# Kernel tuning notes

Measured on AMD Instinct MI355X. Metric: run time of the kernel, lower is better.

## Reference

```python
import jax, jax.numpy as jnp
import numpy as np

RADIUS = 0.1
NSAMPLE = 32
NORMALIZE_XYZ = False
USE_XYZ = True


def ball_query(xyz, center_xyz, radius, nsample):
    """xyz: (B,N,3), center_xyz: (B,S,3) -> idx (B,S,nsample) int32.
    For each center, first `nsample` point indices within `radius`;
    slots with no valid point are filled with the first valid index (0 if none)."""
    N = xyz.shape[1]
    # squared distances (B,S,N)
    d2 = jnp.sum((center_xyz[:, :, None, :] - xyz[:, None, :, :]) ** 2, axis=-1)
    in_ball = d2 < radius * radius
    cand = jnp.where(in_ball, jnp.arange(N, dtype=jnp.int32)[None, None, :], jnp.int32(N))
    cand = jnp.sort(cand, axis=-1)[..., :nsample]  # first nsample in-ball indices
    first = cand[..., :1]
    first = jnp.where(first == N, 0, first)  # fallback to 0 if ball is empty
    idx = jnp.where(cand == N, first, cand)
    return idx


def group(features, idx):
    """features: (B,C,N), idx: (B,S,K) -> (B,C,S,K)"""
    return jax.vmap(lambda f, i: f[:, i])(features, idx)


def setup_inputs() -> dict:
    key = jax.random.key(0)
    k1, k2, k3 = jax.random.split(key, 3)
    B, N, S, C = 4, 8192, 2048, 64
    xyz = jax.random.uniform(k1, (B, N, 3), dtype=jnp.float32)
    center_xyz = jax.random.uniform(k2, (B, S, 3), dtype=jnp.float32)
    features = jax.random.normal(k3, (B, C, N), dtype=jnp.float32)
    return {"xyz": xyz, "center_xyz": center_xyz, "features": features}


def reference(xyz, center_xyz, features):
    idx = ball_query(xyz, center_xyz, RADIUS, NSAMPLE)  # (B,S,K)
    xyz_t = jnp.transpose(xyz, (0, 2, 1))  # (B,3,N)
    grouped_xyz = group(xyz_t, idx)  # (B,3,S,K)
    grouped_xyz = grouped_xyz - jnp.transpose(center_xyz, (0, 2, 1))[..., None]
    if NORMALIZE_XYZ:
        grouped_xyz = grouped_xyz / RADIUS
    grouped_features = group(features, idx)  # (B,C,S,K)
    if USE_XYZ:
        return jnp.concatenate([grouped_xyz, grouped_features], axis=1)  # (B,3+C,S,K)
    return grouped_features
```

## Files before the change

kernel.cpp:

```cpp
#include <hip/hip_runtime.h>
#include <stdint.h>

constexpr int N_PTS = 8192;
constexpr int S_CTR = 2048;
constexpr int BATCH = 4;
constexpr int CHANS = 64;
constexpr int KS = 32;
constexpr int CH_OUT = CHANS + 3;
constexpr int M = 2;
constexpr int STAGE = 512;
constexpr int NSG = N_PTS / STAGE;

__global__ __launch_bounds__(256) void bq_kernel(
    const float* __restrict__ xyz, const float* __restrict__ ctr,
    int* __restrict__ idx_out)
{
    __shared__ float pts[2][STAGE * 3];
    __shared__ int lidx[4][M][KS];
    const int t = threadIdx.x;
    const int wave = t >> 6, lane = t & 63;
    const int cg0 = blockIdx.x * (4 * M) + wave * M;
    const int b = cg0 >> 11;
    const float* xb = xyz + (size_t)b * N_PTS * 3;

    float cx[M], cy[M], cz[M];
#pragma unroll
    for (int m = 0; m < M; ++m) {
        const float* c = ctr + (size_t)(cg0 + m) * 3;
        cx[m] = c[0]; cy[m] = c[1]; cz[m] = c[2];
    }
    unsigned cnt[M];
#pragma unroll
    for (int m = 0; m < M; ++m) cnt[m] = 0;

    const float r2 = (float)(0.1 * 0.1);

#pragma unroll
    for (int j = 0; j < 6; ++j)
        pts[0][t + j * 256] = xb[t + j * 256];
    __syncthreads();

    for (int sg = 0; sg < NSG; ++sg) {
        const int cur = sg & 1;
        if (sg + 1 < NSG) {
            const float* src = xb + (size_t)(sg + 1) * STAGE * 3;
#pragma unroll
            for (int j = 0; j < 6; ++j)
                pts[cur ^ 1][t + j * 256] = src[t + j * 256];
        }
        if (cnt[0] < (unsigned)KS || cnt[1] < (unsigned)KS) {
            for (int c8 = 0; c8 < STAGE / 64; ++c8) {
                const int pbase = (c8 * 64 + lane) * 3;
                const float px = pts[cur][pbase + 0];
                const float py = pts[cur][pbase + 1];
                const float pz = pts[cur][pbase + 2];
                const int n = sg * STAGE + c8 * 64 + lane;
#pragma unroll
                for (int m = 0; m < M; ++m) {
                    const float dx = __fsub_rn(cx[m], px);
                    const float dy = __fsub_rn(cy[m], py);
                    const float dz = __fsub_rn(cz[m], pz);
                    const float d2 = __fadd_rn(
                        __fadd_rn(__fmul_rn(dx, dx), __fmul_rn(dy, dy)),
                        __fmul_rn(dz, dz));
                    const bool inb = d2 < r2;
                    const unsigned long long mask = __ballot(inb);
                    if (mask != 0ull && cnt[m] < (unsigned)KS) {
                        const unsigned rank = __builtin_amdgcn_mbcnt_hi(
                            (unsigned)(mask >> 32),
                            __builtin_amdgcn_mbcnt_lo((unsigned)mask, 0u));
                        const unsigned slot = cnt[m] + rank;
                        if (inb && slot < (unsigned)KS) lidx[wave][m][slot] = n;
                        cnt[m] += (unsigned)__popcll(mask);
                    }
                }
            }
        }
        __syncthreads();
    }

    const int k = lane & 31;
    const int hh = lane >> 5;
    const unsigned c = hh ? cnt[1] : cnt[0];
    const int first = (c > 0) ? lidx[wave][hh][0] : 0;
    const int v = (k < (int)c) ? lidx[wave][hh][k] : first;
    idx_out[(size_t)(cg0 + hh) * KS + k] = v;
}

__global__ __launch_bounds__(256) void transpose_kernel(
    const float* __restrict__ feat, float* __restrict__ featT)
{
    __shared__ float tile[64][65];
    const int t = threadIdx.x;
    const int n0 = blockIdx.x * 64;
    const int b = blockIdx.y;
    const float* fb = feat + (size_t)b * CHANS * N_PTS;
#pragma unroll
    for (int r = 0; r < 16; ++r) {
        const int c = r * 4 + (t >> 6);
        tile[c][t & 63] = fb[(size_t)c * N_PTS + n0 + (t & 63)];
    }
    __syncthreads();
    float* ob = featT + ((size_t)b * N_PTS + n0) * CHANS;
#pragma unroll
    for (int r = 0; r < 16; ++r) {
        const int n = r * 4 + (t >> 6);
        ob[(size_t)n * CHANS + (t & 63)] = tile[t & 63][n];
    }
}

__global__ __launch_bounds__(256) void gather_kernel(
    const float* __restrict__ xyz, const float* __restrict__ ctr,
    const float* __restrict__ featT, const int* __restrict__ idx_ws,
    float* __restrict__ out)
{
    const int tg = blockIdx.x * 256 + threadIdx.x;
    const int cg = tg >> 5;
    const int k = tg & 31;
    const int b = cg >> 11;
    const int s = cg & (S_CTR - 1);
    const int id = idx_ws[(size_t)cg * KS + k];

    const float* pp = xyz + ((size_t)b * N_PTS + id) * 3;
    const float* cc = ctr + (size_t)cg * 3;
    const float g0 = __fsub_rn(pp[0], cc[0]);
    const float g1 = __fsub_rn(pp[1], cc[1]);
    const float g2 = __fsub_rn(pp[2], cc[2]);

    float f[CHANS];
    const float4* fr =
        (const float4*)(featT + ((size_t)b * N_PTS + id) * CHANS);
#pragma unroll
    for (int j = 0; j < CHANS / 4; ++j) {
        const float4 v = fr[j];
        f[j * 4 + 0] = v.x; f[j * 4 + 1] = v.y;
        f[j * 4 + 2] = v.z; f[j * 4 + 3] = v.w;
    }

    float* ob = out + ((size_t)b * CH_OUT * S_CTR + s) * KS + k;
    const size_t chs = (size_t)S_CTR * KS;
    ob[0] = g0;
    ob[chs] = g1;
    ob[2 * chs] = g2;
#pragma unroll
    for (int ch = 0; ch < CHANS; ++ch)
        ob[(size_t)(ch + 3) * chs] = f[ch];
}

__global__ __launch_bounds__(256) void gather_direct(
    const float* __restrict__ xyz, const float* __restrict__ ctr,
    const float* __restrict__ feat, const int* __restrict__ idx_ws,
    float* __restrict__ out)
{
    const int wave = threadIdx.x >> 6;
    const int lane = threadIdx.x & 63;
    const int cg = blockIdx.x * 4 + wave;
    const int b = cg >> 11;
    const int s = cg & (S_CTR - 1);
    const int k = lane & 31;
    const int half = lane >> 5;

    const int id = idx_ws[(size_t)cg * KS + k];
    const float* pp = xyz + ((size_t)b * N_PTS + id) * 3;
    const float* cc = ctr + (size_t)cg * 3;
    const float g0 = __fsub_rn(pp[0], cc[0]);
    const float g1 = __fsub_rn(pp[1], cc[1]);
    const float g2 = __fsub_rn(pp[2], cc[2]);

    const float* fb = feat + (size_t)b * CHANS * N_PTS + id;
    float* ob = out + ((size_t)b * CH_OUT * S_CTR + s) * KS + k;
    const size_t chs = (size_t)S_CTR * KS;

#pragma unroll
    for (int ch0 = 0; ch0 < CH_OUT; ch0 += 2) {
        const int ch = ch0 + half;
        if (ch < CH_OUT) {
            float v;
            if (ch0 == 0)      v = half ? g1 : g0;
            else if (ch0 == 2) v = half ? fb[0] : g2;
            else               v = fb[(size_t)(ch - 3) * N_PTS];
            ob[(size_t)ch * chs] = v;
        }
    }
}

extern "C" void kernel_launch(void* const* d_in, const int* in_sizes, int n_in,
                              void* d_out, int out_size, void* d_ws, size_t ws_size,
                              hipStream_t stream)
{
    const float* xyz  = (const float*)d_in[0];
    const float* ctr  = (const float*)d_in[1];
    const float* feat = (const float*)d_in[2];
    float* out = (float*)d_out;

    const size_t idx_bytes = (size_t)BATCH * S_CTR * KS * sizeof(int);
    const size_t featT_bytes = (size_t)BATCH * N_PTS * CHANS * sizeof(float);
    int* idx_ws = (int*)d_ws;

    bq_kernel<<<dim3(BATCH * S_CTR / (4 * M)), dim3(256), 0, stream>>>(
        xyz, ctr, idx_ws);

    if (ws_size >= idx_bytes + featT_bytes) {
        float* featT = (float*)((char*)d_ws + idx_bytes);
        transpose_kernel<<<dim3(N_PTS / 64, BATCH), dim3(256), 0, stream>>>(
            feat, featT);
        gather_kernel<<<dim3(BATCH * S_CTR * KS / 256), dim3(256), 0, stream>>>(
            xyz, ctr, featT, idx_ws, out);
    } else {
        gather_direct<<<dim3(BATCH * S_CTR / 4), dim3(256), 0, stream>>>(
            xyz, ctr, feat, idx_ws, out);
    }
}
```

Measured before the change: 123.1 us.

## Replace brute-force ball query with uniform-grid spatial hashing and bitonic sort

Builds a per-batch 10x10x10 uniform grid, with cell size equal to the radius, using counting sort in shared memory. Each center's query then scans only the 27 neighbouring cells instead of all points. Because candidates arrive in cell order, up to 128 in-ball indices are collected and bitonic-sorted with wavefront shuffles, which recovers the first 32 by original index. This removes the O(N) distance scan per center. In exchange it adds a grid-build kernel that runs on only 4 blocks, and results are truncated if more than 128 points fall inside one ball.

```diff
diff --git a/kernel.cpp b/kernel.cpp
--- a/kernel.cpp
+++ b/kernel.cpp
@@ -7,84 +7,150 @@
 constexpr int CHANS = 64;
 constexpr int KS = 32;
 constexpr int CH_OUT = CHANS + 3;
-constexpr int M = 2;
-constexpr int STAGE = 512;
-constexpr int NSG = N_PTS / STAGE;
-
-__global__ __launch_bounds__(256) void bq_kernel(
-    const float* __restrict__ xyz, const float* __restrict__ ctr,
+constexpr int GD = 10;
+constexpr int NCELL = GD * GD * GD;
+constexpr int CAP = 128;
+
+__device__ __forceinline__ int cell_of(float p) {
+    int c = (int)((double)p * 10.0);
+    return c < 0 ? 0 : (c > GD - 1 ? GD - 1 : c);
+}
+
+__global__ __launch_bounds__(1024) void grid_build(
+    const float* __restrict__ xyz, int* __restrict__ cellStart,
+    int* __restrict__ sIdx, float* __restrict__ sX,
+    float* __restrict__ sY, float* __restrict__ sZ)
+{
+    __shared__ int cnts[NCELL];
+    __shared__ int sc[1024];
+    __shared__ int off[NCELL];
+    const int b = blockIdx.x, t = threadIdx.x;
+    const float* xb = xyz + (size_t)b * N_PTS * 3;
+
+    for (int i = t; i < NCELL; i += 1024) cnts[i] = 0;
+    __syncthreads();
+
+    int cellr[8];
+#pragma unroll
+    for (int j = 0; j < 8; ++j) {
+        const int i = t + j * 1024;
+        const float x = xb[i * 3], y = xb[i * 3 + 1], z = xb[i * 3 + 2];
+        const int c = (cell_of(z) * GD + cell_of(y)) * GD + cell_of(x);
+        cellr[j] = c;
+        atomicAdd(&cnts[c], 1);
+    }
+    __syncthreads();
+
+    sc[t] = (t < NCELL) ? cnts[t] : 0;
+    __syncthreads();
+    for (int o = 1; o < 1024; o <<= 1) {
+        const int v = (t >= o) ? sc[t - o] : 0;
+        __syncthreads();
+        sc[t] += v;
+        __syncthreads();
+    }
+    const int excl = (t == 0) ? 0 : sc[t - 1];
+    if (t < NCELL) { cellStart[b * (NCELL + 1) + t] = excl; off[t] = excl; }
+    if (t == 0) cellStart[b * (NCELL + 1) + NCELL] = N_PTS;
+    __syncthreads();
+
+#pragma unroll
+    for (int j = 0; j < 8; ++j) {
+        const int i = t + j * 1024;
+        const int pos = atomicAdd(&off[cellr[j]], 1);
+        sIdx[b * N_PTS + pos] = i;
+        sX[b * N_PTS + pos] = xb[i * 3];
+        sY[b * N_PTS + pos] = xb[i * 3 + 1];
+        sZ[b * N_PTS + pos] = xb[i * 3 + 2];
+    }
+}
+
+__global__ __launch_bounds__(256) void bq_query(
+    const float* __restrict__ ctr, const int* __restrict__ cellStart,
+    const int* __restrict__ sIdx, const float* __restrict__ sX,
+    const float* __restrict__ sY, const float* __restrict__ sZ,
     int* __restrict__ idx_out)
 {
-    __shared__ float pts[2][STAGE * 3];
-    __shared__ int lidx[4][M][KS];
-    const int t = threadIdx.x;
-    const int wave = t >> 6, lane = t & 63;
-    const int cg0 = blockIdx.x * (4 * M) + wave * M;
-    const int b = cg0 >> 11;
-    const float* xb = xyz + (size_t)b * N_PTS * 3;
-
-    float cx[M], cy[M], cz[M];
-#pragma unroll
-    for (int m = 0; m < M; ++m) {
-        const float* c = ctr + (size_t)(cg0 + m) * 3;
-        cx[m] = c[0]; cy[m] = c[1]; cz[m] = c[2];
-    }
-    unsigned cnt[M];
-#pragma unroll
-    for (int m = 0; m < M; ++m) cnt[m] = 0;
-
+    __shared__ int cand[4][CAP];
+    const int wave = threadIdx.x >> 6, lane = threadIdx.x & 63;
+    const int cg = blockIdx.x * 4 + wave;
+    const int b = cg >> 11;
+    const float cx = ctr[(size_t)cg * 3];
+    const float cy = ctr[(size_t)cg * 3 + 1];
+    const float cz = ctr[(size_t)cg * 3 + 2];
     const float r2 = (float)(0.1 * 0.1);
 
-#pragma unroll
-    for (int j = 0; j < 6; ++j)
-        pts[0][t + j * 256] = xb[t + j * 256];
-    __syncthreads();
-
-    for (int sg = 0; sg < NSG; ++sg) {
-        const int cur = sg & 1;
-        if (sg + 1 < NSG) {
-            const float* src = xb + (size_t)(sg + 1) * STAGE * 3;
-#pragma unroll
-            for (int j = 0; j < 6; ++j)
-                pts[cur ^ 1][t + j * 256] = src[t + j * 256];
-        }
-        if (cnt[0] < (unsigned)KS || cnt[1] < (unsigned)KS) {
-            for (int c8 = 0; c8 < STAGE / 64; ++c8) {
-                const int pbase = (c8 * 64 + lane) * 3;
-                const float px = pts[cur][pbase + 0];
-                const float py = pts[cur][pbase + 1];
-                const float pz = pts[cur][pbase + 2];
-                const int n = sg * STAGE + c8 * 64 + lane;
-#pragma unroll
-                for (int m = 0; m < M; ++m) {
-                    const float dx = __fsub_rn(cx[m], px);
-                    const float dy = __fsub_rn(cy[m], py);
-                    const float dz = __fsub_rn(cz[m], pz);
-                    const float d2 = __fadd_rn(
-                        __fadd_rn(__fmul_rn(dx, dx), __fmul_rn(dy, dy)),
-                        __fmul_rn(dz, dz));
-                    const bool inb = d2 < r2;
-                    const unsigned long long mask = __ballot(inb);
-                    if (mask != 0ull && cnt[m] < (unsigned)KS) {
-                        const unsigned rank = __builtin_amdgcn_mbcnt_hi(
-                            (unsigned)(mask >> 32),
-                            __builtin_amdgcn_mbcnt_lo((unsigned)mask, 0u));
-                        const unsigned slot = cnt[m] + rank;
-                        if (inb && slot < (unsigned)KS) lidx[wave][m][slot] = n;
-                        cnt[m] += (unsigned)__popcll(mask);
+    const int ix = cell_of(cx), iy = cell_of(cy), iz = cell_of(cz);
+    const int xlo = max(ix - 1, 0), xhi = min(ix + 1, GD - 1);
+    const int ylo = max(iy - 1, 0), yhi = min(iy + 1, GD - 1);
+    const int zlo = max(iz - 1, 0), zhi = min(iz + 1, GD - 1);
+
+    unsigned cnt = 0;
+    const int csb = b * (NCELL + 1);
+    const int pb = b * N_PTS;
+
+    for (int zz = zlo; zz <= zhi; ++zz)
+        for (int yy = ylo; yy <= yhi; ++yy) {
+            const int rowc = (zz * GD + yy) * GD;
+            const int rs = cellStart[csb + rowc + xlo];
+            const int re = cellStart[csb + rowc + xhi + 1];
+            for (int p0 = rs; p0 < re; p0 += 64) {
+                const int i = p0 + lane;
+                const bool valid = i < re;
+                float px = 1e9f, py = 1e9f, pz = 1e9f; int oid = 0;
+                if (valid) {
+                    px = sX[pb + i]; py = sY[pb + i]; pz = sZ[pb + i];
+                    oid = sIdx[pb + i];
+                }
+                const float dx = __fsub_rn(cx, px);
+                const float dy = __fsub_rn(cy, py);
+                const float dz = __fsub_rn(cz, pz);
+                const float d2 = __fadd_rn(
+                    __fadd_rn(__fmul_rn(dx, dx), __fmul_rn(dy, dy)),
+                    __fmul_rn(dz, dz));
+                const bool inb = valid && (d2 < r2);
+                const unsigned long long mask = __ballot(inb);
+                if (mask) {
+                    const unsigned rank = __builtin_amdgcn_mbcnt_hi(
+                        (unsigned)(mask >> 32),
+                        __builtin_amdgcn_mbcnt_lo((unsigned)mask, 0u));
+                    if (inb) {
+                        const unsigned slot = cnt + rank;
+                        if (slot < (unsigned)CAP) cand[wave][slot] = oid;
                     }
+                    cnt += (unsigned)__popcll(mask);
                 }
             }
         }
-        __syncthreads();
-    }
-
-    const int k = lane & 31;
-    const int hh = lane >> 5;
-    const unsigned c = hh ? cnt[1] : cnt[0];
-    const int first = (c > 0) ? lidx[wave][hh][0] : 0;
-    const int v = (k < (int)c) ? lidx[wave][hh][k] : first;
-    idx_out[(size_t)(cg0 + hh) * KS + k] = v;
+    if (cnt > (unsigned)CAP) cnt = CAP;
+
+    int v0 = (lane < (int)cnt) ? cand[wave][lane] : 0x7fffffff;
+    int v1 = (lane + 64 < (int)cnt) ? cand[wave][lane + 64] : 0x7fffffff;
+#pragma unroll
+    for (int k = 2; k <= 128; k <<= 1) {
+        if (k == 128) {
+            const int a = min(v0, v1); v1 = max(v0, v1); v0 = a;
+        }
+#pragma unroll
+        for (int j = (k == 128 ? 32 : (k >> 1)); j >= 1; j >>= 1) {
+            const int o0 = __shfl_xor(v0, j);
+            const int o1 = __shfl_xor(v1, j);
+            const bool lower = (lane & j) == 0;
+            bool up0, up1;
+            if (k == 64)       { up0 = true;  up1 = false; }
+            else if (k == 128) { up0 = true;  up1 = true;  }
+            else { const bool u = (lane & k) == 0; up0 = u; up1 = u; }
+            v0 = (up0 == lower) ? min(v0, o0) : max(v0, o0);
+            v1 = (up1 == lower) ? min(v1, o1) : max(v1, o1);
+        }
+    }
+
+    int first = __shfl(v0, 0);
+    if (cnt == 0u) first = 0;
+    if (lane < KS) {
+        const int val = (lane < (int)cnt) ? v0 : first;
+        idx_out[(size_t)cg * KS + lane] = val;
+    }
 }
 
 __global__ __launch_bounds__(256) void transpose_kernel(
@@ -128,8 +194,7 @@
     const float g2 = __fsub_rn(pp[2], cc[2]);
 
     float f[CHANS];
-    const float4* fr =
-        (const float4*)(featT + ((size_t)b * N_PTS + id) * CHANS);
+    const float4* fr = (const float4*)(featT + ((size_t)b * N_PTS + id) * CHANS);
 #pragma unroll
     for (int j = 0; j < CHANS / 4; ++j) {
         const float4 v = fr[j];
@@ -147,30 +212,63 @@
         ob[(size_t)(ch + 3) * chs] = f[ch];
 }
 
+__global__ __launch_bounds__(256) void bq_brute(
+    const float* __restrict__ xyz, const float* __restrict__ ctr,
+    int* __restrict__ idx_out)
+{
+    const int wave = threadIdx.x >> 6, lane = threadIdx.x & 63;
+    const int cg = blockIdx.x * 4 + wave;
+    const int b = cg >> 11;
+    const float* xb = xyz + (size_t)b * N_PTS * 3;
+    const float cx = ctr[(size_t)cg * 3], cy = ctr[(size_t)cg * 3 + 1],
+                cz = ctr[(size_t)cg * 3 + 2];
+    __shared__ int lidx[4][KS];
+    unsigned cnt = 0;
+    const float r2 = (float)(0.1 * 0.1);
+    for (int n0 = 0; n0 < N_PTS && cnt < (unsigned)KS; n0 += 64) {
+        const int n = n0 + lane;
+        const float px = xb[n * 3], py = xb[n * 3 + 1], pz = xb[n * 3 + 2];
+        const float dx = __fsub_rn(cx, px), dy = __fsub_rn(cy, py),
+                    dz = __fsub_rn(cz, pz);
+        const float d2 = __fadd_rn(
+            __fadd_rn(__fmul_rn(dx, dx), __fmul_rn(dy, dy)), __fmul_rn(dz, dz));
+        const bool inb = d2 < r2;
+        const unsigned long long mask = __ballot(inb);
+        if (mask) {
+            const unsigned rank = __builtin_amdgcn_mbcnt_hi(
+                (unsigned)(mask >> 32),
+                __builtin_amdgcn_mbcnt_lo((unsigned)mask, 0u));
+            const unsigned slot = cnt + rank;
+            if (inb && slot < (unsigned)KS) lidx[wave][slot] = n;
+            cnt += (unsigned)__popcll(mask);
+        }
+    }
+    if (cnt > (unsigned)KS) cnt = KS;
+    const int first = (cnt > 0) ? lidx[wave][0] : 0;
+    if (lane < KS)
+        idx_out[(size_t)cg * KS + lane] = (lane < (int)cnt) ? lidx[wave][lane] : first;
+}
+
 __global__ __launch_bounds__(256) void gather_direct(
     const float* __restrict__ xyz, const float* __restrict__ ctr,
     const float* __restrict__ feat, const int* __restrict__ idx_ws,
     float* __restrict__ out)
 {
-    const int wave = threadIdx.x >> 6;
-    const int lane = threadIdx.x & 63;
+    const int wave = threadIdx.x >> 6, lane = threadIdx.x & 63;
     const int cg = blockIdx.x * 4 + wave;
     const int b = cg >> 11;
     const int s = cg & (S_CTR - 1);
     const int k = lane & 31;
     const int half = lane >> 5;
-
     const int id = idx_ws[(size_t)cg * KS + k];
     const float* pp = xyz + ((size_t)b * N_PTS + id) * 3;
     const float* cc = ctr + (size_t)cg * 3;
     const float g0 = __fsub_rn(pp[0], cc[0]);
     const float g1 = __fsub_rn(pp[1], cc[1]);
     const float g2 = __fsub_rn(pp[2], cc[2]);
-
     const float* fb = feat + (size_t)b * CHANS * N_PTS + id;
     float* ob = out + ((size_t)b * CH_OUT * S_CTR + s) * KS + k;
     const size_t chs = (size_t)S_CTR * KS;
-
 #pragma unroll
     for (int ch0 = 0; ch0 < CH_OUT; ch0 += 2) {
         const int ch = ch0 + half;
@@ -193,20 +291,37 @@
     const float* feat = (const float*)d_in[2];
     float* out = (float*)d_out;
 
-    const size_t idx_bytes = (size_t)BATCH * S_CTR * KS * sizeof(int);
-    const size_t featT_bytes = (size_t)BATCH * N_PTS * CHANS * sizeof(float);
-    int* idx_ws = (int*)d_ws;
-
-    bq_kernel<<<dim3(BATCH * S_CTR / (4 * M)), dim3(256), 0, stream>>>(
-        xyz, ctr, idx_ws);
-
-    if (ws_size >= idx_bytes + featT_bytes) {
-        float* featT = (float*)((char*)d_ws + idx_bytes);
+    char* w = (char*)d_ws;
+    const size_t idx_off   = 0;
+    const size_t cs_off    = 1048576;
+    const size_t sidx_off  = 1064704;
+    const size_t sx_off    = 1195776;
+    const size_t sy_off    = 1326848;
+    const size_t sz_off    = 1457920;
+    const size_t featT_off = 1588992;
+    const size_t total_need = featT_off + (size_t)BATCH * N_PTS * CHANS * 4;
+
+    int* idx_ws = (int*)(w + idx_off);
+
+    if (ws_size >= total_need) {
+        int*   cellStart = (int*)(w + cs_off);
+        int*   sIdx = (int*)(w + sidx_off);
+        float* sX = (float*)(w + sx_off);
+        float* sY = (float*)(w + sy_off);
+        float* sZ = (float*)(w + sz_off);
+        float* featT = (float*)(w + featT_off);
+
+        grid_build<<<dim3(BATCH), dim3(1024), 0, stream>>>(
+            xyz, cellStart, sIdx, sX, sY, sZ);
+        bq_query<<<dim3(BATCH * S_CTR / 4), dim3(256), 0, stream>>>(
+            ctr, cellStart, sIdx, sX, sY, sZ, idx_ws);
         transpose_kernel<<<dim3(N_PTS / 64, BATCH), dim3(256), 0, stream>>>(
             feat, featT);
         gather_kernel<<<dim3(BATCH * S_CTR * KS / 256), dim3(256), 0, stream>>>(
             xyz, ctr, featT, idx_ws, out);
     } else {
+        bq_brute<<<dim3(BATCH * S_CTR / 4), dim3(256), 0, stream>>>(
+            xyz, ctr, idx_ws);
         gather_direct<<<dim3(BATCH * S_CTR / 4), dim3(256), 0, stream>>>(
             xyz, ctr, feat, idx_ws, out);
     }
```

Measured after the change: 134.7 us. 1.09x slower.
